# Optimization experiments

Hardware: AMD Instinct MI355X
Metric: run time of the kernel (lower is better)

Reference implementation:

```python
import jax, jax.numpy as jnp
import numpy as np

N_HEADS = 4
NEG_SLOPE = 0.2  # DGL GATConv default leaky_relu slope


def setup_inputs() -> dict:
    key = jax.random.key(0)
    ks = jax.random.split(key, 12)
    N, E = 50000, 800000
    in_dim, time_dim, out_dim = 128, 128, 128
    d_head = out_dim // N_HEADS
    in_total = in_dim + time_dim
    h = jax.random.normal(ks[0], (N, in_dim), jnp.float32)
    time_tensor = jax.random.uniform(ks[1], (E,), jnp.float32)
    src = jax.random.randint(ks[2], (E,), 0, N, jnp.int32)
    dst = jax.random.randint(ks[3], (E,), 0, N, jnp.int32)
    # TimeEncoding: Linear(1, time_dim) with xavier weight, zero bias
    w_t = jax.random.normal(ks[4], (time_dim, 1), jnp.float32) * (6.0 / (1 + time_dim)) ** 0.5
    b_t = jnp.zeros((time_dim,), jnp.float32)
    # GATConv params
    W_fc = jax.random.normal(ks[5], (N_HEADS * d_head, in_total), jnp.float32) * (2.0 / in_total) ** 0.5
    attn_l = jax.random.normal(ks[6], (N_HEADS, d_head), jnp.float32) * 0.1
    attn_r = jax.random.normal(ks[7], (N_HEADS, d_head), jnp.float32) * 0.1
    W_res = jax.random.normal(ks[8], (N_HEADS * d_head, in_total), jnp.float32) * (2.0 / in_total) ** 0.5
    bias = jnp.zeros((N_HEADS * d_head,), jnp.float32)
    return {"h": h, "time_tensor": time_tensor, "src": src, "dst": dst,
            "num_nodes": N, "w_t": w_t, "b_t": b_t, "W_fc": W_fc,
            "attn_l": attn_l, "attn_r": attn_r, "W_res": W_res, "bias": bias}


def reference(h, time_tensor, src, dst, num_nodes, w_t, b_t, W_fc, attn_l, attn_r, W_res, bias):
    N = num_nodes
    E = src.shape[0]
    # Time encoding: cos(W t + b), per edge -> [E, time_dim]
    time_emb = jnp.cos(time_tensor[:, None] * w_t[:, 0][None, :] + b_t[None, :])
    # Mailbox mean of concat([src h, time_emb]) per dst node.
    # mean(concat) == concat(mean, mean), so sum the two halves separately.
    ones = jnp.ones((E,), h.dtype)
    deg = jax.ops.segment_sum(ones, dst, num_segments=N)  # [N]
    sum_h = jax.ops.segment_sum(h[src], dst, num_segments=N)       # [N, in_dim]
    sum_t = jax.ops.segment_sum(time_emb, dst, num_segments=N)     # [N, time_dim]
    inv_deg = 1.0 / jnp.maximum(deg, 1.0)
    h_time = jnp.concatenate([sum_h, sum_t], axis=1) * inv_deg[:, None]  # [N, in+time]
    # GATConv (eval mode, no dropout)
    d_head = W_fc.shape[0] // N_HEADS
    feat = (h_time @ W_fc.T).reshape(N, N_HEADS, d_head)  # [N,H,D]
    el = jnp.sum(feat * attn_l[None], axis=-1)  # [N,H]
    er = jnp.sum(feat * attn_r[None], axis=-1)  # [N,H]
    e = el[src] + er[dst]                        # [E,H]
    e = jnp.where(e > 0, e, NEG_SLOPE * e)
    # edge softmax over incoming edges of each dst node
    m = jax.ops.segment_max(e, dst, num_segments=N)  # [N,H]
    m = jnp.where(jnp.isfinite(m), m, 0.0)
    ex = jnp.exp(e - m[dst])
    denom = jax.ops.segment_sum(ex, dst, num_segments=N)
    a = ex / jnp.maximum(denom[dst], 1e-9)           # [E,H]
    rst = jax.ops.segment_sum(a[:, :, None] * feat[src], dst, num_segments=N)  # [N,H,D]
    res = (h_time @ W_res.T).reshape(N, N_HEADS, d_head)
    out = rst + res + bias.reshape(1, N_HEADS, d_head)
    out = jax.nn.elu(out)
    return out.reshape(N, -1)  # [N, out_dim]
```

## Files before the change

### kernel.cpp

```cpp
#include <hip/hip_runtime.h>
#include <math.h>

#define NH 4
#define NEG_SLOPE 0.2f
#define BKT_SHIFT 8
#define EPB 4096
#define INV2PI 0.15915494309189535f
#define LOG2E  1.4426950408889634f

typedef __attribute__((ext_vector_type(8))) short bf16x8;
typedef __attribute__((ext_vector_type(4))) float f32x4;

__device__ __forceinline__ float blo(unsigned u) { return __uint_as_float(u << 16); }
__device__ __forceinline__ float bhi(unsigned u) { return __uint_as_float(u & 0xFFFF0000u); }
__device__ __forceinline__ unsigned short rne(float f) {
    unsigned u = __float_as_uint(f);
    u += 0x7FFFu + ((u >> 16) & 1u);
    return (unsigned short)(u >> 16);
}
__device__ __forceinline__ unsigned pack2(float a, float b) {
    return (unsigned)rne(a) | ((unsigned)rne(b) << 16);
}

__global__ __launch_bounds__(256) void k_prep(
    const int* __restrict__ dst, int* __restrict__ deg_i, int E,
    const float* __restrict__ h, unsigned* __restrict__ hbu, int n_pairs,
    const float* __restrict__ Wfc, const float* __restrict__ Wres,
    unsigned* __restrict__ wcat,
    const float* __restrict__ w_t, const float* __restrict__ b_t,
    float2* __restrict__ w_s, float2* __restrict__ b_s) {
    int t = blockIdx.x * blockDim.x + threadIdx.x;
    int base = t * 4;
    if (base + 3 < E) {
        int4 d = ((const int4*)dst)[t];
        atomicAdd(deg_i + d.x, 1);
        atomicAdd(deg_i + d.y, 1);
        atomicAdd(deg_i + d.z, 1);
        atomicAdd(deg_i + d.w, 1);
    } else if (base < E) {
        for (int e = base; e < E; e++) atomicAdd(deg_i + dst[e], 1);
    }
    if (t < n_pairs) {
        float2 v = ((const float2*)h)[t];
        hbu[t] = pack2(v.x, v.y);
    }
    if (t < 32768) {
        int col = t >> 7, kk = t & 127;
        const float* srcp = (col < 128) ? (Wfc + (size_t)col * 256)
                                        : (Wres + (size_t)(col - 128) * 256);
        float2 v = ((const float2*)srcp)[kk];
        wcat[t] = pack2(v.x, v.y);
    }
    if (t < 64) {
        float2 wv = ((const float2*)w_t)[t];
        float2 bv = ((const float2*)b_t)[t];
        w_s[t] = make_float2(wv.x * INV2PI, wv.y * INV2PI);
        b_s[t] = make_float2(bv.x * INV2PI, bv.y * INV2PI);
    }
}

__global__ __launch_bounds__(1024) void k_blocksum(const int* __restrict__ deg_i,
                                                   int* __restrict__ partials, int N) {
    __shared__ int wsum[16];
    int tid = threadIdx.x, lane = tid & 63, wid = tid >> 6;
    int i = blockIdx.x * 1024 + tid;
    int v = (i < N) ? deg_i[i] : 0;
#pragma unroll
    for (int off = 32; off > 0; off >>= 1) v += __shfl_xor(v, off, 64);
    if (lane == 0) wsum[wid] = v;
    __syncthreads();
    if (tid == 0) {
        int s = 0;
#pragma unroll
        for (int k = 0; k < 16; k++) s += wsum[k];
        partials[blockIdx.x] = s;
    }
}

__global__ __launch_bounds__(1024) void k_scandown(const int* __restrict__ deg_i,
                                                   const int* __restrict__ partials,
                                                   int* __restrict__ row_start,
                                                   int* __restrict__ bkt_cursor,
                                                   int N, int B) {
    __shared__ int wsum[16];
    __shared__ int s_off;
    int tid = threadIdx.x, lane = tid & 63, wid = tid >> 6;
    if (wid == 0) {
        int pv = (lane < B) ? partials[lane] : 0;
        int px = pv;
#pragma unroll
        for (int off = 1; off < 64; off <<= 1) {
            int y = __shfl_up(px, off, 64);
            if (lane >= off) px += y;
        }
        if (lane == (int)blockIdx.x) s_off = px - pv;
        if (blockIdx.x == 0 && lane == B - 1) row_start[N] = px;
    }
    int i = blockIdx.x * 1024 + tid;
    int v = (i < N) ? deg_i[i] : 0;
    int x = v;
#pragma unroll
    for (int off = 1; off < 64; off <<= 1) {
        int y = __shfl_up(x, off, 64);
        if (lane >= off) x += y;
    }
    if (lane == 63) wsum[wid] = x;
    __syncthreads();
    if (wid == 0 && lane < 16) {
        int s = wsum[lane];
#pragma unroll
        for (int off = 1; off < 16; off <<= 1) {
            int y = __shfl_up(s, off, 64);
            if (lane >= off) s += y;
        }
        wsum[lane] = s;
    }
    __syncthreads();
    if (i < N) {
        int base = s_off + (wid > 0 ? wsum[wid - 1] : 0);
        int excl = base + x - v;
        row_start[i] = excl;
        if ((i & 255) == 0) bkt_cursor[i >> BKT_SHIFT] = excl;
    }
}

__global__ __launch_bounds__(256) void k_binscatter(
    const int* __restrict__ src, const int* __restrict__ dst,
    const float* __restrict__ tt, int* __restrict__ bkt_cursor,
    uint2* __restrict__ staged, int E, int NB) {
    __shared__ int cnt[1024];
    __shared__ int basep[1024];
    int e0 = blockIdx.x * EPB;
    int tid = threadIdx.x;
    for (int b = tid; b < NB; b += 256) cnt[b] = 0;
    __syncthreads();
#pragma unroll
    for (int k = 0; k < EPB / 256; k++) {
        int e = e0 + k * 256 + tid;
        if (e < E) atomicAdd(&cnt[dst[e] >> BKT_SHIFT], 1);
    }
    __syncthreads();
    for (int b = tid; b < NB; b += 256) {
        int c = cnt[b];
        basep[b] = (c > 0) ? atomicAdd(bkt_cursor + b, c) : 0;
        cnt[b] = 0;
    }
    __syncthreads();
#pragma unroll
    for (int k = 0; k < EPB / 256; k++) {
        int e = e0 + k * 256 + tid;
        if (e < E) {
            int d = dst[e];
            int b = d >> BKT_SHIFT;
            int r = atomicAdd(&cnt[b], 1);
            unsigned tq = min((unsigned)(tt[e] * 32768.0f), 32767u);
            staged[basep[b] + r] =
                make_uint2(((unsigned)src[e] << 15) | tq, (unsigned)(d & 255));
        }
    }
}

__global__ __launch_bounds__(256) void k_binsort(
    const uint2* __restrict__ staged, const int* __restrict__ row_start,
    unsigned* __restrict__ est, int N) {
    __shared__ int cur[256];
    int b = blockIdx.x;
    int n0 = b << BKT_SHIFT;
    int n1 = min(n0 + 256, N);
    int tid = threadIdx.x;
    if (tid < n1 - n0) cur[tid] = row_start[n0 + tid];
    __syncthreads();
    int s0 = row_start[n0], s1 = row_start[n1];
    for (int p = s0 + tid; p < s1; p += 256) {
        uint2 v = staged[p];
        int pos = atomicAdd(&cur[v.y], 1);
        est[pos] = v.x;
    }
}

__device__ __forceinline__ void agg_edge(unsigned u, float wgt, const uint4* __restrict__ h4,
                                         int i, float4 wa, float4 wb, float4 ba, float4 bb,
                                         float* aH, float* aT) {
    int s = (int)(u >> 15);
    float t = (float)((u & 0x7FFFu)) * (1.0f / 32768.0f) + (0.5f / 32768.0f);
    uint4 hv = h4[(size_t)s * 16 + i];
    aH[0] += wgt * blo(hv.x); aH[1] += wgt * bhi(hv.x);
    aH[2] += wgt * blo(hv.y); aH[3] += wgt * bhi(hv.y);
    aH[4] += wgt * blo(hv.z); aH[5] += wgt * bhi(hv.z);
    aH[6] += wgt * blo(hv.w); aH[7] += wgt * bhi(hv.w);
    aT[0] += wgt * __builtin_amdgcn_cosf(fmaf(t, wa.x, ba.x));
    aT[1] += wgt * __builtin_amdgcn_cosf(fmaf(t, wa.y, ba.y));
    aT[2] += wgt * __builtin_amdgcn_cosf(fmaf(t, wa.z, ba.z));
    aT[3] += wgt * __builtin_amdgcn_cosf(fmaf(t, wa.w, ba.w));
    aT[4] += wgt * __builtin_amdgcn_cosf(fmaf(t, wb.x, bb.x));
    aT[5] += wgt * __builtin_amdgcn_cosf(fmaf(t, wb.y, bb.y));
    aT[6] += wgt * __builtin_amdgcn_cosf(fmaf(t, wb.z, bb.z));
    aT[7] += wgt * __builtin_amdgcn_cosf(fmaf(t, wb.w, bb.w));
}

__device__ __forceinline__ void attn_edge(unsigned u, bool valid, const uint4* __restrict__ f4,
                                          int i, int hd, const float* __restrict__ el,
                                          float erh, float* acc, float& den) {
    int s = (int)(u >> 15);
    float elh = el[(size_t)s * 4 + hd];
    uint4 fv = f4[(size_t)s * 16 + i];
    float w = elh + erh; w = w > 0.f ? w : NEG_SLOPE * w;
    float ex = valid ? __builtin_amdgcn_exp2f(w) : 0.f;
    acc[0] = fmaf(ex, blo(fv.x), acc[0]); acc[1] = fmaf(ex, bhi(fv.x), acc[1]);
    acc[2] = fmaf(ex, blo(fv.y), acc[2]); acc[3] = fmaf(ex, bhi(fv.y), acc[3]);
    acc[4] = fmaf(ex, blo(fv.z), acc[4]); acc[5] = fmaf(ex, bhi(fv.z), acc[5]);
    acc[6] = fmaf(ex, blo(fv.w), acc[6]); acc[7] = fmaf(ex, bhi(fv.w), acc[7]);
    den += ex;
}

__global__ __launch_bounds__(256) void k_agg(
    const unsigned* __restrict__ hbu, const unsigned* __restrict__ est,
    const int* __restrict__ row_start,
    const float2* __restrict__ w_s, const float2* __restrict__ b_s,
    unsigned* __restrict__ htu, int N) {
    int n = blockIdx.x * 4 + (threadIdx.x >> 6);
    if (n >= N) return;
    int lane = threadIdx.x & 63;
    int g = lane >> 4, i = lane & 15;
    int rs = row_start[n], re = row_start[n + 1];
    const uint4* h4 = (const uint4*)hbu;
    float4 wa = ((const float4*)w_s)[2 * i], wb = ((const float4*)w_s)[2 * i + 1];
    float4 ba = ((const float4*)b_s)[2 * i], bb = ((const float4*)b_s)[2 * i + 1];
    float aH[8] = {}, aT[8] = {};
    for (int e = rs + g; e < re; e += 16) {
        int e1 = e + 4, e2 = e + 8, e3 = e + 12;
        bool v1 = e1 < re, v2 = e2 < re, v3 = e3 < re;
        unsigned u0 = est[e];
        unsigned u1 = est[v1 ? e1 : e];
        unsigned u2 = est[v2 ? e2 : e];
        unsigned u3 = est[v3 ? e3 : e];
        agg_edge(u0, 1.0f, h4, i, wa, wb, ba, bb, aH, aT);
        agg_edge(u1, v1 ? 1.0f : 0.0f, h4, i, wa, wb, ba, bb, aH, aT);
        agg_edge(u2, v2 ? 1.0f : 0.0f, h4, i, wa, wb, ba, bb, aH, aT);
        agg_edge(u3, v3 ? 1.0f : 0.0f, h4, i, wa, wb, ba, bb, aH, aT);
    }
#pragma unroll
    for (int off = 16; off <= 32; off <<= 1) {
#pragma unroll
        for (int k = 0; k < 8; k++) {
            aH[k] += __shfl_xor(aH[k], off, 64);
            aT[k] += __shfl_xor(aT[k], off, 64);
        }
    }
    if (g == 0) {
        int deg = re - rs;
        float idg = (deg > 0) ? 1.0f / (float)deg : 1.0f;
        uint4* ht4 = (uint4*)htu;
        uint4 oh, ot;
        oh.x = pack2(aH[0] * idg, aH[1] * idg);
        oh.y = pack2(aH[2] * idg, aH[3] * idg);
        oh.z = pack2(aH[4] * idg, aH[5] * idg);
        oh.w = pack2(aH[6] * idg, aH[7] * idg);
        ot.x = pack2(aT[0] * idg, aT[1] * idg);
        ot.y = pack2(aT[2] * idg, aT[3] * idg);
        ot.z = pack2(aT[4] * idg, aT[5] * idg);
        ot.w = pack2(aT[6] * idg, aT[7] * idg);
        ht4[(size_t)n * 32 + i]      = oh;
        ht4[(size_t)n * 32 + 16 + i] = ot;
    }
}

__global__ __launch_bounds__(256) void k_gemm(
    const unsigned short* __restrict__ ht, const unsigned short* __restrict__ wcat,
    unsigned short* __restrict__ feat, float* __restrict__ res_out, int N) {
    __shared__ __align__(16) unsigned short As[64 * 264];
    int tid = threadIdx.x;
    int row0 = blockIdx.x * 64;
    const uint4* src4 = (const uint4*)ht;
    for (int idx = tid; idx < 64 * 32; idx += 256) {
        int rl = idx >> 5, c16 = idx & 31;
        int gr = row0 + rl; if (gr >= N) gr = N - 1;
        uint4 v = src4[(size_t)gr * 32 + c16];
        *(uint4*)(As + rl * 264 + c16 * 8) = v;
    }
    __syncthreads();
    int wave = tid >> 6, lane = tid & 63;
    int r = lane & 15, q = lane >> 4;
    int colbase = wave * 64;
    const bf16x8* bbase = (const bf16x8*)wcat + (size_t)(colbase + r) * 32;
    const unsigned short* abase = As + r * 264 + q * 8;
    f32x4 acc[4][4] = {};
#pragma unroll
    for (int ks = 0; ks < 8; ks++) {
        bf16x8 a[4], b[4];
#pragma unroll
        for (int rt = 0; rt < 4; rt++)
            a[rt] = *(const bf16x8*)(abase + rt * (16 * 264) + ks * 32);
#pragma unroll
        for (int ct = 0; ct < 4; ct++)
            b[ct] = bbase[(size_t)ct * (16 * 32) + ks * 4 + q];
#pragma unroll
        for (int rt = 0; rt < 4; rt++)
#pragma unroll
            for (int ct = 0; ct < 4; ct++)
                acc[rt][ct] = __builtin_amdgcn_mfma_f32_16x16x32_bf16(a[rt], b[ct], acc[rt][ct], 0, 0, 0);
    }
#pragma unroll
    for (int rt = 0; rt < 4; rt++) {
        int rb = row0 + rt * 16 + q * 4;
#pragma unroll
        for (int ct = 0; ct < 4; ct++) {
            int col = colbase + ct * 16 + r;
#pragma unroll
            for (int reg = 0; reg < 4; reg++) {
                int row = rb + reg;
                if (row >= N) continue;
                float v = acc[rt][ct][reg];
                if (col < 128) feat[(size_t)row * 128 + col] = rne(v);
                else           res_out[(size_t)row * 128 + (col - 128)] = v;
            }
        }
    }
}

__global__ void k_el_er(const unsigned* __restrict__ featu,
                        const float* __restrict__ attn_l, const float* __restrict__ attn_r,
                        float* __restrict__ el, float* __restrict__ er, int NH4) {
    int t = blockIdx.x * blockDim.x + threadIdx.x;
    if (t >= NH4) return;
    int n = t >> 2, hd = t & 3;
    const unsigned* f = featu + (size_t)n * 64 + hd * 16;
    const float2* al = (const float2*)(attn_l + hd * 32);
    const float2* ar = (const float2*)(attn_r + hd * 32);
    float sl = 0.f, sr = 0.f;
#pragma unroll
    for (int i = 0; i < 16; i++) {
        unsigned u = f[i];
        float f0 = blo(u), f1 = bhi(u);
        float2 a = al[i], b = ar[i];
        sl = fmaf(f0, a.x, fmaf(f1, a.y, sl));
        sr = fmaf(f0, b.x, fmaf(f1, b.y, sr));
    }
    el[t] = sl * LOG2E;
    er[t] = sr * LOG2E;
}

__global__ __launch_bounds__(256) void k_attn(
    const unsigned* __restrict__ est, const int* __restrict__ row_start,
    const float* __restrict__ el, const float* __restrict__ er,
    const unsigned* __restrict__ featu, const float* __restrict__ bias,
    float* __restrict__ out, int N) {
    int n = blockIdx.x * 4 + (threadIdx.x >> 6);
    if (n >= N) return;
    int lane = threadIdx.x & 63;
    int g = lane >> 4, i = lane & 15;
    int hd = i >> 2;
    int rs = row_start[n], re = row_start[n + 1];
    float erh = er[(size_t)n * 4 + hd];
    const uint4* f4 = (const uint4*)featu;
    float acc[8] = {};
    float den = 0.f;
    for (int e = rs + g; e < re; e += 16) {
        int e1 = e + 4, e2 = e + 8, e3 = e + 12;
        bool v1 = e1 < re, v2 = e2 < re, v3 = e3 < re;
        unsigned u0 = est[e];
        unsigned u1 = est[v1 ? e1 : e];
        unsigned u2 = est[v2 ? e2 : e];
        unsigned u3 = est[v3 ? e3 : e];
        attn_edge(u0, true, f4, i, hd, el, erh, acc, den);
        attn_edge(u1, v1, f4, i, hd, el, erh, acc, den);
        attn_edge(u2, v2, f4, i, hd, el, erh, acc, den);
        attn_edge(u3, v3, f4, i, hd, el, erh, acc, den);
    }
#pragma unroll
    for (int off = 16; off <= 32; off <<= 1) {
#pragma unroll
        for (int k = 0; k < 8; k++) acc[k] += __shfl_xor(acc[k], off, 64);
        den += __shfl_xor(den, off, 64);
    }
    if (g == 0) {
        float id = 1.0f / fmaxf(den, 1e-9f);
        float* op = out + (size_t)n * 128 + i * 8;
        const float* bp = bias + i * 8;
        float4 o0 = ((const float4*)op)[0], o1 = ((const float4*)op)[1];
        float4 b0 = ((const float4*)bp)[0], b1 = ((const float4*)bp)[1];
        float4 r0, r1;
        r0.x = fmaf(acc[0], id, o0.x + b0.x);
        r0.y = fmaf(acc[1], id, o0.y + b0.y);
        r0.z = fmaf(acc[2], id, o0.z + b0.z);
        r0.w = fmaf(acc[3], id, o0.w + b0.w);
        r1.x = fmaf(acc[4], id, o1.x + b1.x);
        r1.y = fmaf(acc[5], id, o1.y + b1.y);
        r1.z = fmaf(acc[6], id, o1.z + b1.z);
        r1.w = fmaf(acc[7], id, o1.w + b1.w);
        r0.x = r0.x > 0.f ? r0.x : (__expf(r0.x) - 1.0f);
        r0.y = r0.y > 0.f ? r0.y : (__expf(r0.y) - 1.0f);
        r0.z = r0.z > 0.f ? r0.z : (__expf(r0.z) - 1.0f);
        r0.w = r0.w > 0.f ? r0.w : (__expf(r0.w) - 1.0f);
        r1.x = r1.x > 0.f ? r1.x : (__expf(r1.x) - 1.0f);
        r1.y = r1.y > 0.f ? r1.y : (__expf(r1.y) - 1.0f);
        r1.z = r1.z > 0.f ? r1.z : (__expf(r1.z) - 1.0f);
        r1.w = r1.w > 0.f ? r1.w : (__expf(r1.w) - 1.0f);
        ((float4*)op)[0] = r0;
        ((float4*)op)[1] = r1;
    }
}

extern "C" void kernel_launch(void* const* d_in, const int* in_sizes, int n_in,
                              void* d_out, int out_size, void* d_ws, size_t ws_size,
                              hipStream_t stream) {
    const float* h     = (const float*)d_in[0];
    const float* tt    = (const float*)d_in[1];
    const int*   src   = (const int*)d_in[2];
    const int*   dst   = (const int*)d_in[3];
    const float* w_t   = (const float*)d_in[5];
    const float* b_t   = (const float*)d_in[6];
    const float* W_fc  = (const float*)d_in[7];
    const float* al    = (const float*)d_in[8];
    const float* ar    = (const float*)d_in[9];
    const float* W_res = (const float*)d_in[10];
    const float* bias  = (const float*)d_in[11];

    int N = in_sizes[0] / 128;
    int E = in_sizes[1];
    int B = (N + 1023) / 1024;
    int NB = (N + 255) >> BKT_SHIFT;

    char* ws = (char*)d_ws;
    size_t off = 0;
    auto alloc = [&](size_t bytes) { void* p = ws + off; off = (off + bytes + 15) & ~(size_t)15; return p; };
    unsigned* htu     = (unsigned*)alloc((size_t)N * 128 * 4);
    unsigned* hbu     = (unsigned*)alloc((size_t)N * 64 * 4);
    unsigned* featu   = (unsigned*)alloc((size_t)N * 64 * 4);
    unsigned* wcat    = (unsigned*)alloc(32768 * 4);
    float2*   w_s     = (float2*)alloc(64 * 8);
    float2*   b_s     = (float2*)alloc(64 * 8);
    float*    el      = (float*)alloc((size_t)N * NH * 4);
    float*    er      = (float*)alloc((size_t)N * NH * 4);
    int*      deg_i   = (int*)alloc((size_t)N * 4);
    int*      row_st  = (int*)alloc((size_t)(N + 1) * 4);
    int*      bkt_cur = (int*)alloc((size_t)NB * 4);
    int*      parts   = (int*)alloc((size_t)B * 4);
    unsigned* est     = (unsigned*)alloc((size_t)E * 4);
    uint2*    staged  = (uint2*)featu;

    hipMemsetAsync(deg_i, 0, (size_t)N * 4, stream);

    int prep_n = N * 64;
    hipLaunchKernelGGL(k_prep, dim3((prep_n + 255) / 256), dim3(256), 0, stream,
                       dst, deg_i, E, h, hbu, prep_n, W_fc, W_res, wcat,
                       w_t, b_t, w_s, b_s);
    hipLaunchKernelGGL(k_blocksum, dim3(B), dim3(1024), 0, stream, deg_i, parts, N);
    hipLaunchKernelGGL(k_scandown, dim3(B), dim3(1024), 0, stream,
                       deg_i, parts, row_st, bkt_cur, N, B);
    hipLaunchKernelGGL(k_binscatter, dim3((E + EPB - 1) / EPB), dim3(256), 0, stream,
                       src, dst, tt, bkt_cur, staged, E, NB);
    hipLaunchKernelGGL(k_binsort, dim3(NB), dim3(256), 0, stream,
                       staged, row_st, est, N);
    hipLaunchKernelGGL(k_agg, dim3((N + 3) / 4), dim3(256), 0, stream,
                       hbu, est, row_st, w_s, b_s, htu, N);
    hipLaunchKernelGGL(k_gemm, dim3((N + 63) / 64), dim3(256), 0, stream,
                       (const unsigned short*)htu, (const unsigned short*)wcat,
                       (unsigned short*)featu, (float*)d_out, N);
    hipLaunchKernelGGL(k_el_er, dim3((N * NH + 255) / 256), dim3(256), 0, stream,
                       featu, al, ar, el, er, N * NH);
    hipLaunchKernelGGL(k_attn, dim3((N + 3) / 4), dim3(256), 0, stream,
                       est, row_st, el, er, featu, bias, (float*)d_out, N);
}
```

Baseline: 278.6 us.

## Replace per-node degree atomics and node scan with bucket histogram and in-sort row offsets

Replaces the global per-node degree atomics and the two-kernel 50K-element scan with a per-block shared-memory bucket histogram (196 buckets), a single-block bucket scan, and computation of per-node row offsets inside the bin-sort kernel from a local count and scan. This removes 800K global atomics and the large scan passes, at the cost of an extra read pass over staged edges in binsort. The code relies on NB fitting in 256 threads (N up to 65536) and on the bucket and node counts fitting in those shared arrays.

New measurement: 252.2 us. -9.5%, faster.

```diff
diff --git a/kernel.cpp b/kernel.cpp
--- a/kernel.cpp
+++ b/kernel.cpp
@@ -5,6 +5,7 @@
 #define NEG_SLOPE 0.2f
 #define BKT_SHIFT 8
 #define EPB 4096
+#define CBLK 8192
 #define INV2PI 0.15915494309189535f
 #define LOG2E  1.4426950408889634f
 
@@ -23,23 +24,12 @@
 }
 
 __global__ __launch_bounds__(256) void k_prep(
-    const int* __restrict__ dst, int* __restrict__ deg_i, int E,
     const float* __restrict__ h, unsigned* __restrict__ hbu, int n_pairs,
     const float* __restrict__ Wfc, const float* __restrict__ Wres,
     unsigned* __restrict__ wcat,
     const float* __restrict__ w_t, const float* __restrict__ b_t,
     float2* __restrict__ w_s, float2* __restrict__ b_s) {
     int t = blockIdx.x * blockDim.x + threadIdx.x;
-    int base = t * 4;
-    if (base + 3 < E) {
-        int4 d = ((const int4*)dst)[t];
-        atomicAdd(deg_i + d.x, 1);
-        atomicAdd(deg_i + d.y, 1);
-        atomicAdd(deg_i + d.z, 1);
-        atomicAdd(deg_i + d.w, 1);
-    } else if (base < E) {
-        for (int e = base; e < E; e++) atomicAdd(deg_i + dst[e], 1);
-    }
     if (t < n_pairs) {
         float2 v = ((const float2*)h)[t];
         hbu[t] = pack2(v.x, v.y);
@@ -59,45 +49,41 @@
     }
 }
 
-__global__ __launch_bounds__(1024) void k_blocksum(const int* __restrict__ deg_i,
-                                                   int* __restrict__ partials, int N) {
-    __shared__ int wsum[16];
+__global__ __launch_bounds__(256) void k_bktcount(
+    const int* __restrict__ dst, int* __restrict__ bkt_cnt, int E, int NB) {
+    __shared__ int cnt[256];
+    int tid = threadIdx.x;
+    cnt[tid] = 0;
+    __syncthreads();
+    int q0 = (blockIdx.x * CBLK) >> 2;
+#pragma unroll
+    for (int k = 0; k < CBLK / 1024; k++) {
+        int qi = q0 + k * 256 + tid;
+        int base = qi * 4;
+        if (base + 3 < E) {
+            int4 d = ((const int4*)dst)[qi];
+            atomicAdd(&cnt[d.x >> BKT_SHIFT], 1);
+            atomicAdd(&cnt[d.y >> BKT_SHIFT], 1);
+            atomicAdd(&cnt[d.z >> BKT_SHIFT], 1);
+            atomicAdd(&cnt[d.w >> BKT_SHIFT], 1);
+        } else {
+            for (int e = base; e < E; e++) atomicAdd(&cnt[dst[e] >> BKT_SHIFT], 1);
+        }
+    }
+    __syncthreads();
+    if (tid < NB) {
+        int c = cnt[tid];
+        if (c) atomicAdd(bkt_cnt + tid, c);
+    }
+}
+
+__global__ __launch_bounds__(256) void k_bktscan(
+    const int* __restrict__ bkt_cnt, int* __restrict__ bkt_start,
+    int* __restrict__ bkt_cursor, int* __restrict__ row_start,
+    int NB, int E, int N) {
+    __shared__ int wsum[4];
     int tid = threadIdx.x, lane = tid & 63, wid = tid >> 6;
-    int i = blockIdx.x * 1024 + tid;
-    int v = (i < N) ? deg_i[i] : 0;
-#pragma unroll
-    for (int off = 32; off > 0; off >>= 1) v += __shfl_xor(v, off, 64);
-    if (lane == 0) wsum[wid] = v;
-    __syncthreads();
-    if (tid == 0) {
-        int s = 0;
-#pragma unroll
-        for (int k = 0; k < 16; k++) s += wsum[k];
-        partials[blockIdx.x] = s;
-    }
-}
-
-__global__ __launch_bounds__(1024) void k_scandown(const int* __restrict__ deg_i,
-                                                   const int* __restrict__ partials,
-                                                   int* __restrict__ row_start,
-                                                   int* __restrict__ bkt_cursor,
-                                                   int N, int B) {
-    __shared__ int wsum[16];
-    __shared__ int s_off;
-    int tid = threadIdx.x, lane = tid & 63, wid = tid >> 6;
-    if (wid == 0) {
-        int pv = (lane < B) ? partials[lane] : 0;
-        int px = pv;
-#pragma unroll
-        for (int off = 1; off < 64; off <<= 1) {
-            int y = __shfl_up(px, off, 64);
-            if (lane >= off) px += y;
-        }
-        if (lane == (int)blockIdx.x) s_off = px - pv;
-        if (blockIdx.x == 0 && lane == B - 1) row_start[N] = px;
-    }
-    int i = blockIdx.x * 1024 + tid;
-    int v = (i < N) ? deg_i[i] : 0;
+    int v = (tid < NB) ? bkt_cnt[tid] : 0;
     int x = v;
 #pragma unroll
     for (int off = 1; off < 64; off <<= 1) {
@@ -106,22 +92,15 @@
     }
     if (lane == 63) wsum[wid] = x;
     __syncthreads();
-    if (wid == 0 && lane < 16) {
-        int s = wsum[lane];
-#pragma unroll
-        for (int off = 1; off < 16; off <<= 1) {
-            int y = __shfl_up(s, off, 64);
-            if (lane >= off) s += y;
-        }
-        wsum[lane] = s;
-    }
-    __syncthreads();
-    if (i < N) {
-        int base = s_off + (wid > 0 ? wsum[wid - 1] : 0);
-        int excl = base + x - v;
-        row_start[i] = excl;
-        if ((i & 255) == 0) bkt_cursor[i >> BKT_SHIFT] = excl;
-    }
+    if (tid == 0) {
+        int s = 0;
+#pragma unroll
+        for (int k = 0; k < 4; k++) { int tk = wsum[k]; wsum[k] = s; s += tk; }
+    }
+    __syncthreads();
+    int excl = wsum[wid] + x - v;
+    if (tid < NB) { bkt_start[tid] = excl; bkt_cursor[tid] = excl; }
+    if (tid == 0) { bkt_start[NB] = E; row_start[N] = E; }
 }
 
 __global__ __launch_bounds__(256) void k_binscatter(
@@ -161,20 +140,44 @@
 }
 
 __global__ __launch_bounds__(256) void k_binsort(
-    const uint2* __restrict__ staged, const int* __restrict__ row_start,
-    unsigned* __restrict__ est, int N) {
+    const uint2* __restrict__ staged, const int* __restrict__ bkt_start,
+    int* __restrict__ row_start, unsigned* __restrict__ est, int N) {
+    __shared__ int cnt[256];
     __shared__ int cur[256];
+    __shared__ int wsum[4];
     int b = blockIdx.x;
     int n0 = b << BKT_SHIFT;
-    int n1 = min(n0 + 256, N);
     int tid = threadIdx.x;
-    if (tid < n1 - n0) cur[tid] = row_start[n0 + tid];
-    __syncthreads();
-    int s0 = row_start[n0], s1 = row_start[n1];
+    cnt[tid] = 0;
+    __syncthreads();
+    int s0 = bkt_start[b], s1 = bkt_start[b + 1];
+    for (int p = s0 + tid; p < s1; p += 256)
+        atomicAdd(&cnt[staged[p].y], 1);
+    __syncthreads();
+    int lane = tid & 63, wid = tid >> 6;
+    int v = cnt[tid];
+    int x = v;
+#pragma unroll
+    for (int off = 1; off < 64; off <<= 1) {
+        int y = __shfl_up(x, off, 64);
+        if (lane >= off) x += y;
+    }
+    if (lane == 63) wsum[wid] = x;
+    __syncthreads();
+    if (tid == 0) {
+        int s = 0;
+#pragma unroll
+        for (int k = 0; k < 4; k++) { int tk = wsum[k]; wsum[k] = s; s += tk; }
+    }
+    __syncthreads();
+    int excl = s0 + wsum[wid] + x - v;
+    cur[tid] = excl;
+    if (n0 + tid < N) row_start[n0 + tid] = excl;
+    __syncthreads();
     for (int p = s0 + tid; p < s1; p += 256) {
-        uint2 v = staged[p];
-        int pos = atomicAdd(&cur[v.y], 1);
-        est[pos] = v.x;
+        uint2 vv = staged[p];
+        int pos = atomicAdd(&cur[vv.y], 1);
+        est[pos] = vv.x;
     }
 }
 
@@ -418,7 +421,6 @@
 
     int N = in_sizes[0] / 128;
     int E = in_sizes[1];
-    int B = (N + 1023) / 1024;
     int NB = (N + 255) >> BKT_SHIFT;
 
     char* ws = (char*)d_ws;
@@ -432,26 +434,26 @@
     float2*   b_s     = (float2*)alloc(64 * 8);
     float*    el      = (float*)alloc((size_t)N * NH * 4);
     float*    er      = (float*)alloc((size_t)N * NH * 4);
-    int*      deg_i   = (int*)alloc((size_t)N * 4);
     int*      row_st  = (int*)alloc((size_t)(N + 1) * 4);
     int*      bkt_cur = (int*)alloc((size_t)NB * 4);
-    int*      parts   = (int*)alloc((size_t)B * 4);
+    int*      bkt_cnt = (int*)alloc((size_t)NB * 4);
+    int*      bkt_sta = (int*)alloc((size_t)(NB + 1) * 4);
     unsigned* est     = (unsigned*)alloc((size_t)E * 4);
     uint2*    staged  = (uint2*)featu;
 
-    hipMemsetAsync(deg_i, 0, (size_t)N * 4, stream);
+    hipMemsetAsync(bkt_cnt, 0, (size_t)NB * 4, stream);
 
     int prep_n = N * 64;
     hipLaunchKernelGGL(k_prep, dim3((prep_n + 255) / 256), dim3(256), 0, stream,
-                       dst, deg_i, E, h, hbu, prep_n, W_fc, W_res, wcat,
-                       w_t, b_t, w_s, b_s);
-    hipLaunchKernelGGL(k_blocksum, dim3(B), dim3(1024), 0, stream, deg_i, parts, N);
-    hipLaunchKernelGGL(k_scandown, dim3(B), dim3(1024), 0, stream,
-                       deg_i, parts, row_st, bkt_cur, N, B);
+                       h, hbu, prep_n, W_fc, W_res, wcat, w_t, b_t, w_s, b_s);
+    hipLaunchKernelGGL(k_bktcount, dim3((E + CBLK - 1) / CBLK), dim3(256), 0, stream,
+                       dst, bkt_cnt, E, NB);
+    hipLaunchKernelGGL(k_bktscan, dim3(1), dim3(256), 0, stream,
+                       bkt_cnt, bkt_sta, bkt_cur, row_st, NB, E, N);
     hipLaunchKernelGGL(k_binscatter, dim3((E + EPB - 1) / EPB), dim3(256), 0, stream,
                        src, dst, tt, bkt_cur, staged, E, NB);
     hipLaunchKernelGGL(k_binsort, dim3(NB), dim3(256), 0, stream,
-                       staged, row_st, est, N);
+                       staged, bkt_sta, row_st, est, N);
     hipLaunchKernelGGL(k_agg, dim3((N + 3) / 4), dim3(256), 0, stream,
                        hbu, est, row_st, w_s, b_s, htu, N);
     hipLaunchKernelGGL(k_gemm, dim3((N + 63) / 64), dim3(256), 0, stream,
```
